# Performance work log

Hardware: AMD Instinct MI355X
Metric: run time of the kernel (lower is better)

## Reference

```python
import jax, jax.numpy as jnp
import numpy as np

B, S, D = 4, 2048, 768
H, DK = 12, 64  # n_heads, head dim (d_k == d_v)
SCALE = 0.02


def setup_inputs() -> dict:
    key = jax.random.key(0)
    ks = jax.random.split(key, 11)
    r = lambda k, shape: jax.random.normal(k, shape, dtype=jnp.float32)
    return {
        "q": r(ks[0], (B, S, D)),
        "k": r(ks[1], (B, S, D)),
        "v": r(ks[2], (B, S, D)),
        "w_q": r(ks[3], (D, H * DK)) * SCALE, "b_q": jnp.zeros((H * DK,), jnp.float32),
        "w_k": r(ks[4], (D, H * DK)) * SCALE, "b_k": jnp.zeros((H * DK,), jnp.float32),
        "w_v": r(ks[5], (D, H * DK)) * SCALE, "b_v": jnp.zeros((H * DK,), jnp.float32),
        "w_o": r(ks[6], (H * DK, D)) * SCALE, "b_o": jnp.zeros((D,), jnp.float32),
    }


def reference(q, k, v, w_q, b_q, w_k, b_k, w_v, b_v, w_o, b_o):
    # project and split heads: [B,S,D] -> [B,H,S,DK]
    split = lambda x: x.reshape(B, S, H, DK).transpose(0, 2, 1, 3)
    qi = split(q @ w_q + b_q)
    ki = split(k @ w_k + b_k)
    vi = split(v @ w_v + b_v)
    # scaled scores [B,H,S,S]
    scores = jnp.einsum("bhqd,bhkd->bhqk", qi, ki) / jnp.sqrt(jnp.float32(DK))
    # causal mask (triu above diagonal -> -inf), same as torch.triu(..., diagonal=1)
    causal = jnp.triu(jnp.ones((S, S), dtype=bool), 1)
    scores = jnp.where(causal, -jnp.inf, scores)
    attn = jax.nn.softmax(scores, axis=-1)  # dropout p=0 -> identity
    out = jnp.einsum("bhqk,bhkd->bhqd", attn, vi)
    out = out.transpose(0, 2, 1, 3).reshape(B, S, H * DK)  # merge heads
    return out @ w_o + b_o
```

## Files before the change

### kernel.cpp

```cpp
#include <hip/hip_runtime.h>

#define NB 4
#define NS 2048
#define ND 768
#define NH 12
#define NDK 64

typedef __bf16 bf16;
typedef __bf16 bf16x8 __attribute__((ext_vector_type(8)));
typedef float f32x4 __attribute__((ext_vector_type(4)));

__device__ inline void gload16(const void* g, void* l) {
    __builtin_amdgcn_global_load_lds((const __attribute__((address_space(1))) void*)g,
                                     (__attribute__((address_space(3))) void*)l, 16, 0, 0);
}

__global__ __launch_bounds__(256) void cvt_kernel(const float* __restrict__ x0, const float* __restrict__ x1,
                                                  const float* __restrict__ x2, bf16* __restrict__ y0,
                                                  bf16* __restrict__ y1, bf16* __restrict__ y2) {
    const float* x = blockIdx.y == 0 ? x0 : blockIdx.y == 1 ? x1 : x2;
    bf16* y        = blockIdx.y == 0 ? y0 : blockIdx.y == 1 ? y1 : y2;
    size_t i = ((size_t)blockIdx.x * 256 + threadIdx.x) * 8;
    f32x4 a = *(const f32x4*)(x + i);
    f32x4 b = *(const f32x4*)(x + i + 4);
    bf16x8 t;
    t[0] = (bf16)a[0]; t[1] = (bf16)a[1]; t[2] = (bf16)a[2]; t[3] = (bf16)a[3];
    t[4] = (bf16)b[0]; t[5] = (bf16)b[1]; t[6] = (bf16)b[2]; t[7] = (bf16)b[3];
    *(bf16x8*)(y + i) = t;
}

__global__ void wtrans_kernel(const float* __restrict__ w0, const float* __restrict__ w1,
                              const float* __restrict__ w2, const float* __restrict__ w3,
                              bf16* __restrict__ t0, bf16* __restrict__ t1,
                              bf16* __restrict__ t2, bf16* __restrict__ t3) {
    const float* w = blockIdx.z == 0 ? w0 : blockIdx.z == 1 ? w1 : blockIdx.z == 2 ? w2 : w3;
    bf16* wt       = blockIdx.z == 0 ? t0 : blockIdx.z == 1 ? t1 : blockIdx.z == 2 ? t2 : t3;
    __shared__ float tile[32][33];
    int k0 = blockIdx.x * 32, n0 = blockIdx.y * 32;
    int tx = threadIdx.x, ty = threadIdx.y;
#pragma unroll
    for (int i = 0; i < 4; ++i) {
        int r = ty + i * 8;
        tile[r][tx] = w[(size_t)(k0 + r) * ND + n0 + tx];
    }
    __syncthreads();
#pragma unroll
    for (int i = 0; i < 4; ++i) {
        int r = ty + i * 8;
        wt[(size_t)(n0 + r) * ND + k0 + tx] = (bf16)tile[tx][r];
    }
}


template <int OUT_MODE>
__device__ inline void gemm_tile(const bf16* __restrict__ A, const bf16* __restrict__ WT,
                                 const float* __restrict__ bias, void* __restrict__ outp,
                                 int rowbase, int colbase) {
    __shared__ bf16 sA[128 * 32];
    __shared__ bf16 sB[128 * 32];
    int lane = threadIdx.x & 63;
    int wave = threadIdx.x >> 6;
    int lr = lane & 15;
    int g = lane >> 4;
    int lk = g * 8;

    f32x4 acc[4][4] = {};

    for (int kt = 0; kt < ND / 32; ++kt) {
#pragma unroll
        for (int c = 0; c < 2; ++c) {
            int slot = wave * 128 + c * 64 + lane;
            int r = slot >> 2;
            int kc = (slot & 3) ^ (r & 3);
            gload16(A + (size_t)(rowbase + r) * ND + kt * 32 + kc * 8, sA + (size_t)(wave * 128 + c * 64) * 8);
            gload16(WT + (size_t)(colbase + r) * ND + kt * 32 + kc * 8, sB + (size_t)(wave * 128 + c * 64) * 8);
        }
        __syncthreads();
        bf16x8 af[4], bfr[4];
#pragma unroll
        for (int mi = 0; mi < 4; ++mi) {
            int row = ((wave >> 1) * 64) + mi * 16 + lr;
            af[mi] = *(const bf16x8*)(sA + row * 32 + ((g ^ (row & 3)) * 8));
        }
#pragma unroll
        for (int ni = 0; ni < 4; ++ni) {
            int col = ((wave & 1) * 64) + ni * 16 + lr;
            bfr[ni] = *(const bf16x8*)(sB + col * 32 + ((g ^ (col & 3)) * 8));
        }
#pragma unroll
        for (int mi = 0; mi < 4; ++mi)
#pragma unroll
            for (int ni = 0; ni < 4; ++ni)
                acc[mi][ni] = __builtin_amdgcn_mfma_f32_16x16x32_bf16(af[mi], bfr[ni], acc[mi][ni], 0, 0, 0);
        __syncthreads();
    }

    int rj = g * 4;
    int wrow = rowbase + (wave >> 1) * 64;
    int wcol = colbase + (wave & 1) * 64;
#pragma unroll
    for (int mi = 0; mi < 4; ++mi) {
#pragma unroll
        for (int ni = 0; ni < 4; ++ni) {
            int col = wcol + ni * 16 + lr;
            float bv = bias[col % ND];
            int h = (col % ND) >> 6, dk = col & 63;
#pragma unroll
            for (int j = 0; j < 4; ++j) {
                int row = wrow + mi * 16 + rj + j;
                float v = acc[mi][ni][j] + bv;
                if (OUT_MODE == 2) {
                    ((float*)outp)[(size_t)row * ND + col] = v;
                } else {
                    int bb = row >> 11, s = row & (NS - 1);
                    if (OUT_MODE == 1)
                        ((bf16*)outp)[(((size_t)bb * NH + h) * NDK + dk) * NS + s] = (bf16)v;
                    else
                        ((bf16*)outp)[(((size_t)bb * NH + h) * NS + s) * NDK + dk] = (bf16)v;
                }
            }
        }
    }
}

__global__ __launch_bounds__(256) void proj_kernel(
    const bf16* __restrict__ Aq, const bf16* __restrict__ Ak, const bf16* __restrict__ Av,
    const bf16* __restrict__ Wq, const bf16* __restrict__ Wk, const bf16* __restrict__ Wv,
    const float* __restrict__ bq, const float* __restrict__ bk, const float* __restrict__ bv,
    bf16* __restrict__ Oq, bf16* __restrict__ Ok, bf16* __restrict__ Ov) {
    int z = blockIdx.z;
    const bf16* A = z == 0 ? Aq : z == 1 ? Ak : Av;
    const bf16* WT = z == 0 ? Wq : z == 1 ? Wk : Wv;
    const float* bias = z == 0 ? bq : z == 1 ? bk : bv;
    bf16* out = z == 0 ? Oq : z == 1 ? Ok : Ov;
    if (z == 2)
        gemm_tile<1>(A, WT, bias, out, blockIdx.x * 128, blockIdx.y * 128);
    else
        gemm_tile<0>(A, WT, bias, out, blockIdx.x * 128, blockIdx.y * 128);
}

__global__ __launch_bounds__(256) void outproj_kernel(
    const bf16* __restrict__ A, const bf16* __restrict__ WT,
    const float* __restrict__ bias, float* __restrict__ out) {
    gemm_tile<2>(A, WT, bias, out, blockIdx.x * 128, blockIdx.y * 128);
}

__global__ __launch_bounds__(256) void attn_kernel(
    const bf16* __restrict__ Qp, const bf16* __restrict__ Kp,
    const bf16* __restrict__ VT, bf16* __restrict__ O) {
    __shared__ char plds[4][4096];
    int lane = threadIdx.x & 63;
    int wave = threadIdx.x >> 6;
    int bh = blockIdx.x;
    int bb = bh / NH, h = bh % NH;
    int qt = gridDim.y - 1 - blockIdx.y;
    int q0 = qt * 128 + wave * 32;
    char* pbase = plds[wave];

    const bf16* Qb = Qp + (size_t)bh * NS * NDK;
    const bf16* Kb = Kp + (size_t)bh * NS * NDK;
    const bf16* Vb = VT + (size_t)bh * NDK * NS;

    int lc = lane & 15;
    int g = lane >> 4;
    int lk = g * 8;
    int rj = g * 4;

    bf16x8 qf[2][2];
#pragma unroll
    for (int qs = 0; qs < 2; ++qs) {
        const bf16* qp = Qb + (size_t)(q0 + qs * 16 + lc) * NDK;
        qf[qs][0] = *(const bf16x8*)(qp + lk);
        qf[qs][1] = *(const bf16x8*)(qp + 32 + lk);
    }

    f32x4 oacc[2][4] = {};
    float lsum[2][4] = {};
    const float scale = 0.125f;
    const int kbmax = (q0 + 31) >> 6;

    bf16x8 kA[4][2], kB[4][2];
    auto load_k = [&](int kb, bf16x8(&kr)[4][2]) {
        const bf16* kp = Kb + (size_t)kb * 64 * NDK;
#pragma unroll
        for (int ks = 0; ks < 4; ++ks) {
            kr[ks][0] = *(const bf16x8*)(kp + (size_t)(ks * 16 + lc) * NDK + lk);
            kr[ks][1] = *(const bf16x8*)(kp + (size_t)(ks * 16 + lc) * NDK + 32 + lk);
        }
    };

    auto body = [&](int kb, bf16x8(&kc)[4][2], bf16x8(&kn)[4][2]) {
        int key0 = kb * 64;
        bf16x8 vr[2][4];
#pragma unroll
        for (int kh = 0; kh < 2; ++kh)
#pragma unroll
            for (int n = 0; n < 4; ++n)
                vr[kh][n] = *(const bf16x8*)(Vb + (size_t)(n * 16 + lc) * NS + key0 + kh * 32 + lk);
        if (kb < kbmax) load_k(kb + 1, kn);

        f32x4 s[2][4] = {};
#pragma unroll
        for (int ks = 0; ks < 4; ++ks) {
            s[0][ks] = __builtin_amdgcn_mfma_f32_16x16x32_bf16(qf[0][0], kc[ks][0], s[0][ks], 0, 0, 0);
            s[1][ks] = __builtin_amdgcn_mfma_f32_16x16x32_bf16(qf[1][0], kc[ks][0], s[1][ks], 0, 0, 0);
            s[0][ks] = __builtin_amdgcn_mfma_f32_16x16x32_bf16(qf[0][1], kc[ks][1], s[0][ks], 0, 0, 0);
            s[1][ks] = __builtin_amdgcn_mfma_f32_16x16x32_bf16(qf[1][1], kc[ks][1], s[1][ks], 0, 0, 0);
        }
        bool needmask = (key0 + 63 > q0);
#pragma unroll
        for (int qs = 0; qs < 2; ++qs)
#pragma unroll
            for (int ks = 0; ks < 4; ++ks)
#pragma unroll
                for (int j = 0; j < 4; ++j) {
                    float p = __expf(s[qs][ks][j] * scale);
                    int qq = qs * 16 + rj + j;
                    if (needmask) {
                        if (key0 + ks * 16 + lc > q0 + qq) p = 0.f;
                    }
                    lsum[qs][j] += p;
                    *(bf16*)(pbase + ((qq * 128 + (ks * 16 + lc) * 2) ^ ((qq & 7) << 4))) = (bf16)p;
                }
        asm volatile("s_waitcnt lgkmcnt(0)" ::: "memory");
        __builtin_amdgcn_sched_barrier(0);
#pragma unroll
        for (int kh = 0; kh < 2; ++kh) {
            bf16x8 pa0 = *(const bf16x8*)(pbase + ((lc * 128 + kh * 64 + g * 16) ^ ((lc & 7) << 4)));
            bf16x8 pa1 = *(const bf16x8*)(pbase + (((16 + lc) * 128 + kh * 64 + g * 16) ^ ((lc & 7) << 4)));
#pragma unroll
            for (int n = 0; n < 4; ++n) {
                oacc[0][n] = __builtin_amdgcn_mfma_f32_16x16x32_bf16(pa0, vr[kh][n], oacc[0][n], 0, 0, 0);
                oacc[1][n] = __builtin_amdgcn_mfma_f32_16x16x32_bf16(pa1, vr[kh][n], oacc[1][n], 0, 0, 0);
            }
        }
    };

    load_k(0, kA);
    int kb = 0;
    while (true) {
        body(kb, kA, kB);
        if (++kb > kbmax) break;
        body(kb, kB, kA);
        if (++kb > kbmax) break;
    }

#pragma unroll
    for (int d = 1; d < 16; d <<= 1)
#pragma unroll
        for (int qs = 0; qs < 2; ++qs)
#pragma unroll
            for (int j = 0; j < 4; ++j)
                lsum[qs][j] += __shfl_xor(lsum[qs][j], d, 64);

#pragma unroll
    for (int qs = 0; qs < 2; ++qs)
#pragma unroll
        for (int j = 0; j < 4; ++j) {
            float inv = 1.0f / lsum[qs][j];
            size_t orow = ((size_t)bb * NS + q0 + qs * 16 + rj + j) * (NH * NDK) + (size_t)h * NDK;
#pragma unroll
            for (int n = 0; n < 4; ++n)
                O[orow + n * 16 + lc] = (bf16)(oacc[qs][n][j] * inv);
        }
}

extern "C" void kernel_launch(void* const* d_in, const int* in_sizes, int n_in,
                              void* d_out, int out_size, void* d_ws, size_t ws_size,
                              hipStream_t stream) {
    const float* q   = (const float*)d_in[0];
    const float* k   = (const float*)d_in[1];
    const float* v   = (const float*)d_in[2];
    const float* w_q = (const float*)d_in[3];
    const float* b_q = (const float*)d_in[4];
    const float* w_k = (const float*)d_in[5];
    const float* b_k = (const float*)d_in[6];
    const float* w_v = (const float*)d_in[7];
    const float* b_v = (const float*)d_in[8];
    const float* w_o = (const float*)d_in[9];
    const float* b_o = (const float*)d_in[10];
    float* out = (float*)d_out;

    char* ws = (char*)d_ws;
    const size_t WT_BYTES = (size_t)ND * ND * 2;
    const size_t PROJ_BYTES = (size_t)NB * NS * NH * NDK * 2;
    bf16* wtq = (bf16*)(ws + 0 * WT_BYTES);
    bf16* wtk = (bf16*)(ws + 1 * WT_BYTES);
    bf16* wtv = (bf16*)(ws + 2 * WT_BYTES);
    bf16* wto = (bf16*)(ws + 3 * WT_BYTES);
    bf16* Qp  = (bf16*)(ws + 4 * WT_BYTES);
    bf16* Kp  = (bf16*)(ws + 4 * WT_BYTES + 1 * PROJ_BYTES);
    bf16* VT  = (bf16*)(ws + 4 * WT_BYTES + 2 * PROJ_BYTES);
    bf16* O   = (bf16*)(ws + 4 * WT_BYTES + 3 * PROJ_BYTES);
    bf16* qb  = (bf16*)(ws + 4 * WT_BYTES + 4 * PROJ_BYTES);
    bf16* kb  = (bf16*)(ws + 4 * WT_BYTES + 5 * PROJ_BYTES);
    bf16* vb  = (bf16*)(ws + 4 * WT_BYTES + 6 * PROJ_BYTES);

    dim3 tb(32, 8);
    wtrans_kernel<<<dim3(24, 24, 4), tb, 0, stream>>>(w_q, w_k, w_v, w_o, wtq, wtk, wtv, wto);
    cvt_kernel<<<dim3(3072, 3), 256, 0, stream>>>(q, k, v, qb, kb, vb);

    proj_kernel<<<dim3(64, 6, 3), 256, 0, stream>>>(qb, kb, vb, wtq, wtk, wtv, b_q, b_k, b_v, Qp, Kp, VT);

    attn_kernel<<<dim3(NB * NH, NS / 128), 256, 0, stream>>>(Qp, Kp, VT, O);

    outproj_kernel<<<dim3(64, 6), 256, 0, stream>>>(O, wto, b_o, out);
}
```

Baseline: 308.1 us.

## Split attention into single-wave blocks and halve outproj row tile

The attention kernel now launches one 64-thread block per 32-query strip (3072 blocks, heaviest strips first) instead of four waves per 128-query block. Each wave is scheduled independently, which should balance causal work and improve occupancy. The output projection uses a 64-row tile, doubling its grid to 768 blocks so the CUs are better filled. A sched_barrier is removed and the bias indexing is simplified; waves no longer share a block, which may cost some K/V reuse through cache.

```diff
diff --git a/kernel.cpp b/kernel.cpp
--- a/kernel.cpp
+++ b/kernel.cpp
@@ -51,35 +51,40 @@
     }
 }
 
-
-template <int OUT_MODE>
+template <int OUT_MODE, int BMI>
 __device__ inline void gemm_tile(const bf16* __restrict__ A, const bf16* __restrict__ WT,
                                  const float* __restrict__ bias, void* __restrict__ outp,
                                  int rowbase, int colbase) {
-    __shared__ bf16 sA[128 * 32];
+    __shared__ bf16 sA[BMI * 32 * 32];
     __shared__ bf16 sB[128 * 32];
     int lane = threadIdx.x & 63;
     int wave = threadIdx.x >> 6;
     int lr = lane & 15;
     int g = lane >> 4;
-    int lk = g * 8;
-
-    f32x4 acc[4][4] = {};
+
+    f32x4 acc[BMI][4] = {};
+    const int ACH = BMI / 2;
 
     for (int kt = 0; kt < ND / 32; ++kt) {
+#pragma unroll
+        for (int c = 0; c < ACH; ++c) {
+            int slot = wave * (ACH * 64) + c * 64 + lane;
+            int r = slot >> 2;
+            int kc = (slot & 3) ^ (r & 3);
+            gload16(A + (size_t)(rowbase + r) * ND + kt * 32 + kc * 8, sA + (size_t)(wave * (ACH * 64) + c * 64) * 8);
+        }
 #pragma unroll
         for (int c = 0; c < 2; ++c) {
             int slot = wave * 128 + c * 64 + lane;
             int r = slot >> 2;
             int kc = (slot & 3) ^ (r & 3);
-            gload16(A + (size_t)(rowbase + r) * ND + kt * 32 + kc * 8, sA + (size_t)(wave * 128 + c * 64) * 8);
             gload16(WT + (size_t)(colbase + r) * ND + kt * 32 + kc * 8, sB + (size_t)(wave * 128 + c * 64) * 8);
         }
         __syncthreads();
-        bf16x8 af[4], bfr[4];
-#pragma unroll
-        for (int mi = 0; mi < 4; ++mi) {
-            int row = ((wave >> 1) * 64) + mi * 16 + lr;
+        bf16x8 af[BMI], bfr[4];
+#pragma unroll
+        for (int mi = 0; mi < BMI; ++mi) {
+            int row = (wave >> 1) * (BMI * 16) + mi * 16 + lr;
             af[mi] = *(const bf16x8*)(sA + row * 32 + ((g ^ (row & 3)) * 8));
         }
 #pragma unroll
@@ -88,7 +93,7 @@
             bfr[ni] = *(const bf16x8*)(sB + col * 32 + ((g ^ (col & 3)) * 8));
         }
 #pragma unroll
-        for (int mi = 0; mi < 4; ++mi)
+        for (int mi = 0; mi < BMI; ++mi)
 #pragma unroll
             for (int ni = 0; ni < 4; ++ni)
                 acc[mi][ni] = __builtin_amdgcn_mfma_f32_16x16x32_bf16(af[mi], bfr[ni], acc[mi][ni], 0, 0, 0);
@@ -96,15 +101,15 @@
     }
 
     int rj = g * 4;
-    int wrow = rowbase + (wave >> 1) * 64;
+    int wrow = rowbase + (wave >> 1) * (BMI * 16);
     int wcol = colbase + (wave & 1) * 64;
 #pragma unroll
-    for (int mi = 0; mi < 4; ++mi) {
+    for (int mi = 0; mi < BMI; ++mi) {
 #pragma unroll
         for (int ni = 0; ni < 4; ++ni) {
             int col = wcol + ni * 16 + lr;
-            float bv = bias[col % ND];
-            int h = (col % ND) >> 6, dk = col & 63;
+            float bv = bias[col];
+            int h = col >> 6, dk = col & 63;
 #pragma unroll
             for (int j = 0; j < 4; ++j) {
                 int row = wrow + mi * 16 + rj + j;
@@ -134,28 +139,28 @@
     const float* bias = z == 0 ? bq : z == 1 ? bk : bv;
     bf16* out = z == 0 ? Oq : z == 1 ? Ok : Ov;
     if (z == 2)
-        gemm_tile<1>(A, WT, bias, out, blockIdx.x * 128, blockIdx.y * 128);
+        gemm_tile<1, 4>(A, WT, bias, out, blockIdx.x * 128, blockIdx.y * 128);
     else
-        gemm_tile<0>(A, WT, bias, out, blockIdx.x * 128, blockIdx.y * 128);
+        gemm_tile<0, 4>(A, WT, bias, out, blockIdx.x * 128, blockIdx.y * 128);
 }
 
 __global__ __launch_bounds__(256) void outproj_kernel(
     const bf16* __restrict__ A, const bf16* __restrict__ WT,
     const float* __restrict__ bias, float* __restrict__ out) {
-    gemm_tile<2>(A, WT, bias, out, blockIdx.x * 128, blockIdx.y * 128);
-}
-
-__global__ __launch_bounds__(256) void attn_kernel(
+    gemm_tile<2, 2>(A, WT, bias, out, blockIdx.x * 64, blockIdx.y * 128);
+}
+
+__global__ __launch_bounds__(64, 3) void attn_kernel(
     const bf16* __restrict__ Qp, const bf16* __restrict__ Kp,
     const bf16* __restrict__ VT, bf16* __restrict__ O) {
-    __shared__ char plds[4][4096];
-    int lane = threadIdx.x & 63;
-    int wave = threadIdx.x >> 6;
-    int bh = blockIdx.x;
+    __shared__ char plds[4096];
+    int lane = threadIdx.x;
+    int id = blockIdx.x;
+    int bh = id % (NB * NH);
+    int qsub = 63 - id / (NB * NH);
     int bb = bh / NH, h = bh % NH;
-    int qt = gridDim.y - 1 - blockIdx.y;
-    int q0 = qt * 128 + wave * 32;
-    char* pbase = plds[wave];
+    int q0 = qsub * 32;
+    char* pbase = plds;
 
     const bf16* Qb = Qp + (size_t)bh * NS * NDK;
     const bf16* Kb = Kp + (size_t)bh * NS * NDK;
@@ -223,7 +228,6 @@
                     *(bf16*)(pbase + ((qq * 128 + (ks * 16 + lc) * 2) ^ ((qq & 7) << 4))) = (bf16)p;
                 }
         asm volatile("s_waitcnt lgkmcnt(0)" ::: "memory");
-        __builtin_amdgcn_sched_barrier(0);
 #pragma unroll
         for (int kh = 0; kh < 2; ++kh) {
             bf16x8 pa0 = *(const bf16x8*)(pbase + ((lc * 128 + kh * 64 + g * 16) ^ ((lc & 7) << 4)));
@@ -302,7 +306,7 @@
 
     proj_kernel<<<dim3(64, 6, 3), 256, 0, stream>>>(qb, kb, vb, wtq, wtk, wtv, b_q, b_k, b_v, Qp, Kp, VT);
 
-    attn_kernel<<<dim3(NB * NH, NS / 128), 256, 0, stream>>>(Qp, Kp, VT, O);
-
-    outproj_kernel<<<dim3(64, 6), 256, 0, stream>>>(O, wto, b_o, out);
-}
+    attn_kernel<<<dim3(64 * NB * NH), 64, 0, stream>>>(Qp, Kp, VT, O);
+
+    outproj_kernel<<<dim3(128, 6), 256, 0, stream>>>(O, wto, b_o, out);
+}
```

Measured after the change: 531.2 us. 1.72x slower.
